# Optimization experiments

Hardware: AMD Instinct MI355X
Metric: run time of the kernel (lower is better)

Reference implementation:

```python
import jax, jax.numpy as jnp
import numpy as np

SCALE = 2
K_UP = 5
K_ENC = 3


def _conv(x, w, b, pad):
    # NCHW conv, OIHW weights
    y = jax.lax.conv_general_dilated(
        x, w, window_strides=(1, 1), padding=((pad, pad), (pad, pad)),
        dimension_numbers=('NCHW', 'OIHW', 'NCHW'))
    return y + b[None, :, None, None]


def setup_inputs() -> dict:
    key = jax.random.key(0)
    k0, k1, k2 = jax.random.split(key, 3)
    b, c, h, w = 4, 256, 64, 64
    c_mid = 64
    n_kernel = SCALE * SCALE * K_UP * K_UP  # 100
    x = jax.random.normal(k0, (b, c, h, w), jnp.float32)
    w1 = jax.random.normal(k1, (c_mid, c, K_ENC, K_ENC), jnp.float32) * 0.02
    b1 = jnp.zeros((c_mid,), jnp.float32)
    w2 = jax.random.normal(k2, (n_kernel, c_mid, 1, 1), jnp.float32) * 0.02
    b2 = jnp.zeros((n_kernel,), jnp.float32)
    return {"x": x, "w1": w1, "b1": b1, "w2": w2, "b2": b2}


def reference(x, w1, b1, w2, b2):
    b, c, h, w = x.shape
    s, k = SCALE, K_UP
    # kernel prediction encoder: 3x3 conv -> ReLU -> 1x1 conv
    feat = jax.nn.relu(_conv(x, w1, b1, K_ENC // 2))
    kern = _conv(feat, w2, b2, 0)                     # (b, s^2*k^2, h, w)
    kern = jax.nn.softmax(kern, axis=1)               # softmax over full channel dim (as in source)
    kern = kern.reshape(b, s * s, k * k, h, w)
    # F.unfold(x, k, padding=k//2) -> (b, c, k^2, h, w); torch ordering: kh major, kw minor
    pad = k // 2
    xp = jnp.pad(x, ((0, 0), (0, 0), (pad, pad), (pad, pad)))
    patches = jnp.stack([xp[:, :, i:i + h, j:j + w]
                         for i in range(k) for j in range(k)], axis=2)  # (b, c, k^2, h, w)
    # per-pixel weighted reassembly: sum over k^2 neighborhood
    out = jnp.einsum('bskhw,bckhw->bschw', kern, patches)  # (b, s^2, c, h, w)
    # view(b, s^2*c, h, w) then pixel_shuffle(scale), exactly matching torch semantics
    out = out.reshape(b, s * s * c, h, w)
    cout = (s * s * c) // (s * s)
    out = out.reshape(b, cout, s, s, h, w)
    out = out.transpose(0, 1, 4, 2, 5, 3).reshape(b, cout, h * s, w * s)
    return out
```

## Files before the change

### kernel.cpp

```cpp
#include <hip/hip_runtime.h>


#define BB 4
#define CC 256
#define HH 64
#define WW 64
#define CMID 64
#define NKCH 100

typedef __bf16 bf16;
typedef __bf16 bf16x8 __attribute__((ext_vector_type(8)));
typedef float f32x4 __attribute__((ext_vector_type(4)));

__device__ __forceinline__ void async_copy16(const void* gsrc, void* ldst) {
    __builtin_amdgcn_global_load_lds(
        (__attribute__((address_space(1))) void*)(void*)gsrc,
        (__attribute__((address_space(3))) void*)ldst, 16, 0, 0);
}

__global__ void k0a_transform(const float* __restrict__ w1, bf16* __restrict__ w1c) {
    int c8 = blockIdx.x;
    int oq = blockIdx.y;
    int tid = threadIdx.x;
    __shared__ __align__(16) float wf[16 * 300];

    for (int i = tid; i < 16 * 72; i += 256) {
        int o = i / 72, r = i % 72;
        *(float4*)&wf[o * 300 + r * 4] =
            *(const float4*)&w1[(size_t)(oq * 16 + o) * 2304 + c8 * 288 + r * 4];
    }
    __syncthreads();

    for (int t = tid; t < 576; t += 256) {
        int o = t & 15, q = (t >> 4) & 3, kk = t >> 6;
        union { bf16 h[8]; uint4 u; } v;
        #pragma unroll
        for (int i8 = 0; i8 < 8; ++i8)
            v.h[i8] = (bf16)wf[o * 300 + (q * 8 + i8) * 9 + kk];
        *(uint4*)&w1c[(size_t)((((c8 * 9 + kk) * 4 + q) * 64) + oq * 16 + o) * 8] = v.u;
    }
}

__global__ __launch_bounds__(512) void k123_fused(const float* __restrict__ x,
        const bf16* __restrict__ w1c, const float* __restrict__ b1,
        const float* __restrict__ w2, const float* __restrict__ b2,
        float* __restrict__ out) {
    int bh = blockIdx.x;
    int b = bh >> 6, h = bh & 63;
    int tid = threadIdx.x;
    int lane = tid & 63, wid = tid >> 6;
    int l15 = lane & 15, quad = lane >> 4;
    int mhalf = wid & 1, nq = wid >> 1;

    __shared__ __align__(16) char smem[122112];
    bf16*  xs0  = (bf16*)smem;
    bf16*  xs1  = (bf16*)(smem + 15872);
    bf16*  wl0  = (bf16*)(smem + 31744);
    bf16*  wl1  = (bf16*)(smem + 68608);
    float* fs   = (float*)(smem + 105472);
    float* kts  = (float*)(smem + 68608);
    float* red  = (float*)smem;

    const float* xb = x + (size_t)b * (CC * HH * WW);

    int ppp[6], rrr[6];
    bool vmask[6];
    #pragma unroll
    for (int j = 0; j < 6; ++j) {
        int task = wid + j * 8;
        ppp[j] = task & 15;
        rrr[j] = task >> 4;
        int hr = h - 1 + rrr[j];
        vmask[j] = (hr >= 0 && hr < HH);
    }

    float fA0[6], fA1[6], fB0[6], fB1[6];
    #define LOADX(C8, F0, F1)                                                    \
        _Pragma("unroll")                                                        \
        for (int j = 0; j < 6; ++j) {                                            \
            if (vmask[j]) {                                                      \
                const float* src = xb + ((size_t)((C8) * 32 + 2 * ppp[j]) * (HH * WW)) \
                                 + (h - 1 + rrr[j]) * WW + lane;                 \
                F0[j] = src[0]; F1[j] = src[HH * WW];                            \
            }                                                                    \
        }
    #define WRITEB(F0, F1, XSDST)                                                \
        _Pragma("unroll")                                                        \
        for (int j = 0; j < 6; ++j) {                                            \
            if (vmask[j]) {                                                      \
                union { bf16 hh[2]; unsigned u; } cv;                            \
                cv.hh[0] = (bf16)F0[j]; cv.hh[1] = (bf16)F1[j];                  \
                *(unsigned*)&(XSDST)[(rrr[j] * 66 + 1 + lane) * 40 + 2 * ppp[j]] = cv.u; \
            }                                                                    \
        }
    #define ACOPY(C8, WDST)                                                      \
        for (int t = wid; t < 36; t += 8)                                        \
            async_copy16(w1c + ((((C8) * 36 + t) << 9) + lane * 8), (void*)&(WDST)[t << 9]);
    #define MFMAS(XSRC, WSRC)                                                    \
        _Pragma("unroll")                                                        \
        for (int kk = 0; kk < 9; ++kk) {                                         \
            int r3 = kk / 3, kw = kk % 3;                                        \
            bf16x8 a0 = *(const bf16x8*)&(WSRC)[((kk * 4 + quad) * 64 + mhalf * 32 + l15) * 8]; \
            bf16x8 a1 = *(const bf16x8*)&(WSRC)[((kk * 4 + quad) * 64 + mhalf * 32 + 16 + l15) * 8]; \
            bf16x8 xv = *(const bf16x8*)&(XSRC)[(r3 * 66 + nq * 16 + l15 + kw) * 40 + quad * 8]; \
            acc0 = __builtin_amdgcn_mfma_f32_16x16x32_bf16(a0, xv, acc0, 0, 0, 0); \
            acc1 = __builtin_amdgcn_mfma_f32_16x16x32_bf16(a1, xv, acc1, 0, 0, 0); \
        }

    for (int i = tid; i < 7936; i += 512) { xs0[i] = (bf16)0.f; xs1[i] = (bf16)0.f; }
    LOADX(0, fA0, fA1)
    ACOPY(0, wl0)
    __syncthreads();
    WRITEB(fA0, fA1, xs0)
    LOADX(1, fB0, fB1)
    __syncthreads();

    f32x4 acc0 = {0.f, 0.f, 0.f, 0.f}, acc1 = {0.f, 0.f, 0.f, 0.f};

    for (int c8 = 0; c8 < 8; c8 += 2) {
        ACOPY(c8 + 1, wl1)
        MFMAS(xs0, wl0)
        WRITEB(fB0, fB1, xs1)
        if (c8 < 6) { LOADX(c8 + 2, fA0, fA1) }
        __syncthreads();
        if (c8 < 6) { ACOPY(c8 + 2, wl0) }
        MFMAS(xs1, wl1)
        if (c8 < 6) { WRITEB(fA0, fA1, xs0) }
        if (c8 < 6) { LOADX(c8 + 3, fB0, fB1) }
        __syncthreads();
    }

    int px = nq * 16 + l15;
    #pragma unroll
    for (int mi = 0; mi < 2; ++mi) {
        int oc0 = mhalf * 32 + mi * 16 + quad * 4;
        float4 bv = *(const float4*)&b1[oc0];
        f32x4 v = mi ? acc1 : acc0;
        fs[(oc0 + 0) * 65 + px] = fmaxf(v[0] + bv.x, 0.f);
        fs[(oc0 + 1) * 65 + px] = fmaxf(v[1] + bv.y, 0.f);
        fs[(oc0 + 2) * 65 + px] = fmaxf(v[2] + bv.z, 0.f);
        fs[(oc0 + 3) * 65 + px] = fmaxf(v[3] + bv.w, 0.f);
    }
    __syncthreads();

    int t8 = tid & 255, h2 = tid >> 8;
    int w3 = t8 & 63, cg3 = t8 >> 6;
    #define XLOAD(P, V)                                                          \
        _Pragma("unroll")                                                        \
        for (int k = 0; k < 5; ++k) {                                            \
            int idx = t8 + k * 256;                                              \
            int u = idx & 15, cc = (idx >> 4) & 15, rr = idx >> 8;               \
            int hr = h - 2 + rr;                                                 \
            V[k] = make_float4(0.f, 0.f, 0.f, 0.f);                              \
            if (hr >= 0 && hr < HH)                                              \
                V[k] = *(const float4*)&x[(((size_t)b * CC + (2 * (P) + h2) * 16 + cc) * HH + hr) * WW + 4 * u]; \
        }
    #define XWRITE(V, TB)                                                        \
        _Pragma("unroll")                                                        \
        for (int k = 0; k < 5; ++k) {                                            \
            int idx = t8 + k * 256;                                              \
            int u = idx & 15, cc = (idx >> 4) & 15, rr = idx >> 8;               \
            int bse = (rr * 4 + (cc >> 2)) * 68;                                 \
            int c = cc & 3;                                                      \
            _Pragma("unroll")                                                    \
            for (int j = 0; j < 4; ++j) {                                        \
                int s = 2 + 4 * u + j;                                           \
                int sw = s ^ ((s >> 3) & 7);                                     \
                (TB)[(bse + sw) * 4 + c] = ((const float*)&V[k])[j];             \
            }                                                                    \
        }
    float4 xst[5];
    XLOAD(0, xst)

    int w = lane;
    int g = wid, s2 = g & 3, ihalf = g >> 2;
    int i0 = ihalf ? 13 : 0;

    float4 fv[16];
    #pragma unroll
    for (int q = 0; q < 16; ++q) {
        fv[q].x = fs[(4 * q + 0) * 65 + w];
        fv[q].y = fs[(4 * q + 1) * 65 + w];
        fv[q].z = fs[(4 * q + 2) * 65 + w];
        fv[q].w = fs[(4 * q + 3) * 65 + w];
    }

    float lg[13];
    #pragma unroll
    for (int ii = 0; ii < 13; ++ii) {
        int idx = i0 + ii;
        bool act = (idx < 25);
        int oc = s2 * 25 + (act ? idx : 0);
        float a = b2[oc];
        const float4* wr = (const float4*)&w2[oc * 64];
        #pragma unroll
        for (int q = 0; q < 16; ++q) {
            float4 wv = wr[q];
            a += fv[q].x * wv.x + fv[q].y * wv.y + fv[q].z * wv.z + fv[q].w * wv.w;
        }
        lg[ii] = act ? a : -1e30f;
    }

    float m = -1e30f;
    #pragma unroll
    for (int ii = 0; ii < 13; ++ii) m = fmaxf(m, lg[ii]);
    red[g * 64 + w] = m;
    __syncthreads();
    m = fmaxf(fmaxf(fmaxf(red[0 * 64 + w], red[1 * 64 + w]),
                    fmaxf(red[2 * 64 + w], red[3 * 64 + w])),
              fmaxf(fmaxf(red[4 * 64 + w], red[5 * 64 + w]),
                    fmaxf(red[6 * 64 + w], red[7 * 64 + w])));
    float ssum = 0.f;
    #pragma unroll
    for (int ii = 0; ii < 13; ++ii) { lg[ii] = __expf(lg[ii] - m); ssum += lg[ii]; }
    red[512 + g * 64 + w] = ssum;
    __syncthreads();
    ssum = ((red[512 + 0 * 64 + w] + red[512 + 1 * 64 + w]) +
            (red[512 + 2 * 64 + w] + red[512 + 3 * 64 + w])) +
           ((red[512 + 4 * 64 + w] + red[512 + 5 * 64 + w]) +
            (red[512 + 6 * 64 + w] + red[512 + 7 * 64 + w]));
    float inv = 1.f / ssum;
    #pragma unroll
    for (int ii = 0; ii < 13; ++ii)
        if (i0 + ii < 25) kts[((i0 + ii) * 64 + w) * 4 + s2] = lg[ii] * inv;
    __syncthreads();


    #pragma unroll
    for (int reg = 0; reg < 4; ++reg) {
        const int tb = (reg == 0) ? 0 : (reg == 1) ? 21760 : (reg == 2) ? 43520 : 94208;
        if (tid < 320) {
            int c = tid & 3, q = (tid >> 2) & 3, rg = tid >> 4;
            int slot = (q < 2) ? q : (q + 64);
            ((float*)(smem + tb))[(rg * 68 + slot) * 4 + c] = 0.f;
        }
    }

    float* tb0 = (float*)(smem + (h2 ? 21760 : 0));
    float* tb1 = (float*)(smem + (h2 ? 94208 : 43520));

    int swk[5];
    #pragma unroll
    for (int kw = 0; kw < 5; ++kw) {
        int s = w3 + kw;
        swk[kw] = s ^ ((s >> 3) & 7);
    }

    XWRITE(xst, tb0)
    __syncthreads();

    for (int p = 0; p < 8; ++p) {
        if (p < 7) { XLOAD(p + 1, xst) }
        float* T = (p & 1) ? tb1 : tb0;
        f32x4 a0 = {0.f,0.f,0.f,0.f}, a1 = {0.f,0.f,0.f,0.f};
        f32x4 a2 = {0.f,0.f,0.f,0.f}, a3 = {0.f,0.f,0.f,0.f};
        #pragma unroll
        for (int r = 0; r < 5; ++r) {
            #pragma unroll
            for (int kw = 0; kw < 5; ++kw) {
                f32x4 kvv = *(const f32x4*)&kts[((r * 5 + kw) * 64 + w3) * 4];
                f32x4 xv = *(const f32x4*)&T[((r * 4 + cg3) * 68 + swk[kw]) * 4];
                a0 += kvv.x * xv;
                a1 += kvv.y * xv;
                a2 += kvv.z * xv;
                a3 += kvv.w * xv;
            }
        }
        int cq = (2 * p + h2) * 4 + cg3;
        f32x4 accs[4] = {a0, a1, a2, a3};
        #pragma unroll
        for (int s = 0; s < 4; ++s) {
            size_t base = (((size_t)b * 256 + s * 64 + cq) * 128 + 2 * h) * 128 + 2 * w3;
            *(float2*)&out[base]       = make_float2(accs[s][0], accs[s][1]);
            *(float2*)&out[base + 128] = make_float2(accs[s][2], accs[s][3]);
        }
        if (p < 7) {
            float* Tnext = (p & 1) ? tb0 : tb1;
            XWRITE(xst, Tnext)
        }
        __syncthreads();
    }
    #undef LOADX
    #undef WRITEB
    #undef ACOPY
    #undef MFMAS
    #undef XLOAD
    #undef XWRITE
}

extern "C" void kernel_launch(void* const* d_in, const int* in_sizes, int n_in,
                              void* d_out, int out_size, void* d_ws, size_t ws_size,
                              hipStream_t stream) {
    const float* x  = (const float*)d_in[0];
    const float* w1 = (const float*)d_in[1];
    const float* b1 = (const float*)d_in[2];
    const float* w2 = (const float*)d_in[3];
    const float* b2 = (const float*)d_in[4];
    float* out = (float*)d_out;

    bf16* w1c = (bf16*)d_ws;

    k0a_transform<<<dim3(8, 4), 256, 0, stream>>>(w1, w1c);
    k123_fused<<<dim3(BB * HH), 512, 0, stream>>>(x, w1c, b1, w2, b2, out);
}
```

Baseline: 129.9 us.

## Compute 1x1 kernel-prediction conv with bf16 MFMA and hoist x loads earlier

Replaces the per-thread scalar FP32 dot products for the 1x1 conv (w2 applied to 64-channel features) with bf16 MFMA tiles. The features are stored as bf16 in LDS and w2 is pre-converted into an MFMA-friendly layout in the transform kernel. Logits are staged through LDS before the softmax. The global x loads in the main conv loop are also issued before the MFMA block to hide latency. This cuts VALU work and LDS traffic but adds bf16 rounding to the logits and an extra barrier.

```diff
diff --git a/kernel.cpp b/kernel.cpp
--- a/kernel.cpp
+++ b/kernel.cpp
@@ -18,7 +18,8 @@
         (__attribute__((address_space(3))) void*)ldst, 16, 0, 0);
 }
 
-__global__ void k0a_transform(const float* __restrict__ w1, bf16* __restrict__ w1c) {
+__global__ void k0a_transform(const float* __restrict__ w1, const float* __restrict__ w2,
+                              bf16* __restrict__ w1c, bf16* __restrict__ w2c) {
     int c8 = blockIdx.x;
     int oq = blockIdx.y;
     int tid = threadIdx.x;
@@ -39,11 +40,21 @@
             v.h[i8] = (bf16)wf[o * 300 + (q * 8 + i8) * 9 + kk];
         *(uint4*)&w1c[(size_t)((((c8 * 9 + kk) * 4 + q) * 64) + oq * 16 + o) * 8] = v.u;
     }
+
+    if (c8 == 0 && oq == 0) {
+        for (int i = tid; i < 7168; i += 256) {
+            int i8 = i & 7;
+            int oc = (i >> 3) % 112;
+            int kq = (i >> 3) / 112;
+            int ic = (kq >> 2) * 32 + (kq & 3) * 8 + i8;
+            w2c[i] = (oc < NKCH) ? (bf16)w2[oc * 64 + ic] : (bf16)0.f;
+        }
+    }
 }
 
 __global__ __launch_bounds__(512) void k123_fused(const float* __restrict__ x,
-        const bf16* __restrict__ w1c, const float* __restrict__ b1,
-        const float* __restrict__ w2, const float* __restrict__ b2,
+        const bf16* __restrict__ w1c, const bf16* __restrict__ w2c,
+        const float* __restrict__ b1, const float* __restrict__ b2,
         float* __restrict__ out) {
     int bh = blockIdx.x;
     int b = bh >> 6, h = bh & 63;
@@ -52,12 +63,13 @@
     int l15 = lane & 15, quad = lane >> 4;
     int mhalf = wid & 1, nq = wid >> 1;
 
-    __shared__ __align__(16) char smem[122112];
+    __shared__ __align__(16) char smem[115968];
     bf16*  xs0  = (bf16*)smem;
     bf16*  xs1  = (bf16*)(smem + 15872);
     bf16*  wl0  = (bf16*)(smem + 31744);
     bf16*  wl1  = (bf16*)(smem + 68608);
-    float* fs   = (float*)(smem + 105472);
+    bf16*  fsb  = (bf16*)(smem + 105472);
+    float* ls   = (float*)(smem + 31744);
     float* kts  = (float*)(smem + 68608);
     float* red  = (float*)smem;
 
@@ -119,14 +131,14 @@
 
     for (int c8 = 0; c8 < 8; c8 += 2) {
         ACOPY(c8 + 1, wl1)
+        if (c8 < 6) { LOADX(c8 + 2, fA0, fA1) }
         MFMAS(xs0, wl0)
         WRITEB(fB0, fB1, xs1)
-        if (c8 < 6) { LOADX(c8 + 2, fA0, fA1) }
         __syncthreads();
         if (c8 < 6) { ACOPY(c8 + 2, wl0) }
+        if (c8 < 6) { LOADX(c8 + 3, fB0, fB1) }
         MFMAS(xs1, wl1)
         if (c8 < 6) { WRITEB(fA0, fA1, xs0) }
-        if (c8 < 6) { LOADX(c8 + 3, fB0, fB1) }
         __syncthreads();
     }
 
@@ -136,10 +148,12 @@
         int oc0 = mhalf * 32 + mi * 16 + quad * 4;
         float4 bv = *(const float4*)&b1[oc0];
         f32x4 v = mi ? acc1 : acc0;
-        fs[(oc0 + 0) * 65 + px] = fmaxf(v[0] + bv.x, 0.f);
-        fs[(oc0 + 1) * 65 + px] = fmaxf(v[1] + bv.y, 0.f);
-        fs[(oc0 + 2) * 65 + px] = fmaxf(v[2] + bv.z, 0.f);
-        fs[(oc0 + 3) * 65 + px] = fmaxf(v[3] + bv.w, 0.f);
+        union { bf16 hh[4]; unsigned long long u; } o;
+        o.hh[0] = (bf16)fmaxf(v[0] + bv.x, 0.f);
+        o.hh[1] = (bf16)fmaxf(v[1] + bv.y, 0.f);
+        o.hh[2] = (bf16)fmaxf(v[2] + bv.z, 0.f);
+        o.hh[3] = (bf16)fmaxf(v[3] + bv.w, 0.f);
+        *(unsigned long long*)&fsb[px * 72 + oc0] = o.u;
     }
     __syncthreads();
 
@@ -172,18 +186,35 @@
     float4 xst[5];
     XLOAD(0, xst)
 
+    if (wid < 7) {
+        f32x4 lacc0 = {0.f,0.f,0.f,0.f}, lacc1 = {0.f,0.f,0.f,0.f};
+        f32x4 lacc2 = {0.f,0.f,0.f,0.f}, lacc3 = {0.f,0.f,0.f,0.f};
+        #pragma unroll
+        for (int kk = 0; kk < 2; ++kk) {
+            bf16x8 a = *(const bf16x8*)&w2c[(((kk * 4 + quad) * 112) + wid * 16 + l15) * 8];
+            bf16x8 bf0 = *(const bf16x8*)&fsb[( 0 + l15) * 72 + kk * 32 + quad * 8];
+            bf16x8 bf1 = *(const bf16x8*)&fsb[(16 + l15) * 72 + kk * 32 + quad * 8];
+            bf16x8 bf2 = *(const bf16x8*)&fsb[(32 + l15) * 72 + kk * 32 + quad * 8];
+            bf16x8 bf3 = *(const bf16x8*)&fsb[(48 + l15) * 72 + kk * 32 + quad * 8];
+            lacc0 = __builtin_amdgcn_mfma_f32_16x16x32_bf16(a, bf0, lacc0, 0, 0, 0);
+            lacc1 = __builtin_amdgcn_mfma_f32_16x16x32_bf16(a, bf1, lacc1, 0, 0, 0);
+            lacc2 = __builtin_amdgcn_mfma_f32_16x16x32_bf16(a, bf2, lacc2, 0, 0, 0);
+            lacc3 = __builtin_amdgcn_mfma_f32_16x16x32_bf16(a, bf3, lacc3, 0, 0, 0);
+        }
+        f32x4 laccs[4] = {lacc0, lacc1, lacc2, lacc3};
+        #pragma unroll
+        for (int nt = 0; nt < 4; ++nt)
+            #pragma unroll
+            for (int j = 0; j < 4; ++j) {
+                int oc = wid * 16 + quad * 4 + j;
+                if (oc < NKCH) ls[oc * 64 + nt * 16 + l15] = laccs[nt][j];
+            }
+    }
+    __syncthreads();
+
     int w = lane;
     int g = wid, s2 = g & 3, ihalf = g >> 2;
     int i0 = ihalf ? 13 : 0;
-
-    float4 fv[16];
-    #pragma unroll
-    for (int q = 0; q < 16; ++q) {
-        fv[q].x = fs[(4 * q + 0) * 65 + w];
-        fv[q].y = fs[(4 * q + 1) * 65 + w];
-        fv[q].z = fs[(4 * q + 2) * 65 + w];
-        fv[q].w = fs[(4 * q + 3) * 65 + w];
-    }
 
     float lg[13];
     #pragma unroll
@@ -191,14 +222,7 @@
         int idx = i0 + ii;
         bool act = (idx < 25);
         int oc = s2 * 25 + (act ? idx : 0);
-        float a = b2[oc];
-        const float4* wr = (const float4*)&w2[oc * 64];
-        #pragma unroll
-        for (int q = 0; q < 16; ++q) {
-            float4 wv = wr[q];
-            a += fv[q].x * wv.x + fv[q].y * wv.y + fv[q].z * wv.z + fv[q].w * wv.w;
-        }
-        lg[ii] = act ? a : -1e30f;
+        lg[ii] = act ? (ls[oc * 64 + w] + b2[oc]) : -1e30f;
     }
 
     float m = -1e30f;
@@ -224,7 +248,6 @@
     for (int ii = 0; ii < 13; ++ii)
         if (i0 + ii < 25) kts[((i0 + ii) * 64 + w) * 4 + s2] = lg[ii] * inv;
     __syncthreads();
-
 
     #pragma unroll
     for (int reg = 0; reg < 4; ++reg) {
@@ -298,8 +321,10 @@
     const float* b2 = (const float*)d_in[4];
     float* out = (float*)d_out;
 
-    bf16* w1c = (bf16*)d_ws;
-
-    k0a_transform<<<dim3(8, 4), 256, 0, stream>>>(w1, w1c);
-    k123_fused<<<dim3(BB * HH), 512, 0, stream>>>(x, w1c, b1, w2, b2, out);
+    char* wsb = (char*)d_ws;
+    bf16* w1c = (bf16*)wsb;
+    bf16* w2c = (bf16*)(wsb + 294912);
+
+    k0a_transform<<<dim3(8, 4), 256, 0, stream>>>(w1, w2, w1c, w2c);
+    k123_fused<<<dim3(BB * HH), 512, 0, stream>>>(x, w1c, w2c, b1, b2, out);
 }
```

Result: faster. 122.7 us (-5.5%).
